# Optimization experiments

Hardware: AMD Instinct MI355X
Metric: run time of the kernel (lower is better)

The kernel has to match this reference:

```python
import jax, jax.numpy as jnp
import numpy as np

S, C, H, D = 4096, 2048, 16, 128  # seq, channels, heads, head_dim
EPS = 1.1920929e-07  # torch F.rms_norm default eps = finfo(float32).eps


def setup_inputs() -> dict:
    key = jax.random.key(0)
    ks = jax.random.split(key, 12)
    w = 0.02
    return {
        "x": jax.random.normal(ks[0], (S, C), dtype=jnp.float32),
        "rope": jax.random.normal(ks[1], (S, 1, D // 2, 2, 2), dtype=jnp.float32),
        "Wq": jax.random.normal(ks[2], (C, C), dtype=jnp.float32) * w,
        "bq": jnp.zeros((C,), dtype=jnp.float32),
        "Wk": jax.random.normal(ks[3], (C, C), dtype=jnp.float32) * w,
        "bk": jnp.zeros((C,), dtype=jnp.float32),
        "Wv": jax.random.normal(ks[4], (C, C), dtype=jnp.float32) * w,
        "bv": jnp.zeros((C,), dtype=jnp.float32),
        "qn_w": jnp.ones((D,), dtype=jnp.float32),
        "kn_w": jnp.ones((D,), dtype=jnp.float32),
        "Wo": jax.random.normal(ks[5], (C, C), dtype=jnp.float32) * w,
        "bo": jnp.zeros((C,), dtype=jnp.float32),
    }


def _rms_norm(x, weight):
    # RMSNorm over last dim, as F.rms_norm
    inv = jax.lax.rsqrt(jnp.mean(x * x, axis=-1, keepdims=True) + EPS)
    return x * inv * weight


def _apply_rotary(x, rope):
    # x: [S, H, D]; rope: [S, 1, D//2, 2, 2]
    s, h, d = x.shape
    x_ = x.reshape(s, h, d // 2, 1, 2)
    out = (rope * x_).sum(axis=-1)  # [S, H, D//2, 2]
    return out.reshape(s, h, d)


def reference(x, rope, Wq, bq, Wk, bk, Wv, bv, qn_w, kn_w, Wo, bo):
    # QKV projections -> [S, H, D]
    q = (x @ Wq.T + bq).reshape(S, H, D)
    k = (x @ Wk.T + bk).reshape(S, H, D)
    v = (x @ Wv.T + bv).reshape(S, H, D)
    # RMSNorm on q/k per head_dim
    q = _rms_norm(q, qn_w)
    k = _rms_norm(k, kn_w)
    # Custom rotary (table-driven 2x2 rotation)
    q = _apply_rotary(q, rope)
    k = _apply_rotary(k, rope)
    # Dense scaled dot-product attention over seq, per head
    scale = 1.0 / jnp.sqrt(jnp.asarray(D, dtype=q.dtype))
    scores = jnp.einsum("shd,thd->hst", q, k) * scale  # [H, S, S]
    probs = jax.nn.softmax(scores, axis=-1)
    out = jnp.einsum("hst,thd->shd", probs, v).reshape(S, C)
    return out @ Wo.T + bo
```

## Files before the change

kernel.cpp:

```cpp
#include <hip/hip_runtime.h>

#define S 4096
#define C 2048
#define H 16
#define D 128
#define EPS 1.1920929e-07f
#define QSCALE (0.08838834764831845f * 1.4426950408889634f)
#define BN 64
#define NT (S / BN)

typedef __attribute__((ext_vector_type(8))) short short8;
typedef __attribute__((ext_vector_type(4))) float f32x4;
typedef __attribute__((ext_vector_type(4))) unsigned int uint4v;

#if __has_builtin(__builtin_amdgcn_exp2f)
#define EXP2F __builtin_amdgcn_exp2f
#else
#define EXP2F exp2f
#endif

__device__ __forceinline__ unsigned short f2bf(float f) {
  unsigned int u = __builtin_bit_cast(unsigned int, f);
  u += 0x7fff + ((u >> 16) & 1);
  return (unsigned short)(u >> 16);
}
__device__ __forceinline__ float bf2f(unsigned short v) {
  unsigned int u = ((unsigned int)v) << 16;
  return __builtin_bit_cast(float, u);
}
__device__ __forceinline__ unsigned int pkbf(float a, float b) {
  return (unsigned int)f2bf(a) | ((unsigned int)f2bf(b) << 16);
}
__device__ __forceinline__ unsigned int pkbf_trunc(float a, float b) {
  return __builtin_amdgcn_perm(__builtin_bit_cast(unsigned int, b),
                               __builtin_bit_cast(unsigned int, a), 0x07060302);
}
__device__ __forceinline__ void gld16(const unsigned short* g, unsigned short* l) {
  __builtin_amdgcn_global_load_lds(
      (const __attribute__((address_space(1))) unsigned int*)g,
      (__attribute__((address_space(3))) unsigned int*)l, 16, 0, 0);
}
__device__ __forceinline__ short8 mk_a(unsigned int a, unsigned int b,
                                       unsigned int c, unsigned int d) {
  uint4v u;
  u[0] = a; u[1] = b; u[2] = c; u[3] = d;
  return __builtin_bit_cast(short8, u);
}

__global__ void cvt_kernel(const float* __restrict__ src,
                           unsigned short* __restrict__ dst, int n) {
  int i = (blockIdx.x * 256 + threadIdx.x) * 4;
  if (i >= n) return;
  float4 v = *(const float4*)(src + i);
  ushort4 o;
  o.x = f2bf(v.x); o.y = f2bf(v.y); o.z = f2bf(v.z); o.w = f2bf(v.w);
  *(ushort4*)(dst + i) = o;
}
__global__ void cvtw_kernel(const float* __restrict__ w0, const float* __restrict__ w1,
                            const float* __restrict__ w2, const float* __restrict__ w3,
                            unsigned short* __restrict__ dst) {
  const float* srcs[4] = {w0, w1, w2, w3};
  const float* src = srcs[blockIdx.y];
  int i = (blockIdx.x * 256 + threadIdx.x) * 4;
  float4 v = *(const float4*)(src + i);
  ushort4 o;
  o.x = f2bf(v.x); o.y = f2bf(v.y); o.z = f2bf(v.z); o.w = f2bf(v.w);
  *(ushort4*)(dst + (size_t)blockIdx.y * C * C + i) = o;
}
__global__ void bias_concat(const float* __restrict__ bq, const float* __restrict__ bk,
                            const float* __restrict__ bv, float* __restrict__ dst) {
  int i = blockIdx.x * 256 + threadIdx.x;
  const float* s = (i < C) ? bq : ((i < 2 * C) ? bk : bv);
  dst[i] = s[i & (C - 1)];
}

__global__ __launch_bounds__(256) void gemm_bt(const unsigned short* __restrict__ A,
                                               const unsigned short* __restrict__ B,
                                               const float* __restrict__ bias,
                                               float* __restrict__ outf,
                                               unsigned short* __restrict__ qh,
                                               unsigned short* __restrict__ kh,
                                               unsigned short* __restrict__ vt,
                                               int N, int mode) {
  __shared__ __align__(16) unsigned short U[128 * 136];
  unsigned short* Al = U;
  unsigned short* Bl = U + 128 * 64;
  const int t = threadIdx.x, w = t >> 6, lane = t & 63;
  const int lq = lane & 15, quad = lane >> 4;
  const int wm = w & 1, wn = w >> 1;
  const int m0 = blockIdx.y * 128, n0 = blockIdx.x * 128;
  f32x4 acc[4][4] = {};
  float biasv[4];
#pragma unroll
  for (int nt = 0; nt < 4; nt++) biasv[nt] = bias[n0 + wn * 64 + nt * 16 + lq];
  const int sr = lane >> 3, sg = lane & 7;
  for (int k0 = 0; k0 < C; k0 += 64) {
    __syncthreads();
#pragma unroll
    for (int p = 0; p < 4; p++) {
      int row = w * 32 + p * 8 + sr;
      int c = sg ^ (row & 7);
      gld16(A + (size_t)(m0 + row) * C + k0 + c * 8, &Al[(w * 32 + p * 8) * 64]);
      gld16(B + (size_t)(n0 + row) * C + k0 + c * 8, &Bl[(w * 32 + p * 8) * 64]);
    }
    __syncthreads();
#pragma unroll
    for (int ks = 0; ks < 2; ks++) {
      short8 af[4], bf[4];
#pragma unroll
      for (int mt = 0; mt < 4; mt++) {
        int row = wm * 64 + mt * 16 + lq;
        af[mt] = *(const short8*)&Al[row * 64 + ((ks * 4 + quad) ^ (lq & 7)) * 8];
      }
#pragma unroll
      for (int nt = 0; nt < 4; nt++) {
        int row = wn * 64 + nt * 16 + lq;
        bf[nt] = *(const short8*)&Bl[row * 64 + ((ks * 4 + quad) ^ (lq & 7)) * 8];
      }
#pragma unroll
      for (int mt = 0; mt < 4; mt++)
#pragma unroll
        for (int nt = 0; nt < 4; nt++)
          acc[mt][nt] = __builtin_amdgcn_mfma_f32_16x16x32_bf16(af[mt], bf[nt], acc[mt][nt], 0, 0, 0);
    }
  }

  if (mode == 0) {
#pragma unroll
    for (int mt = 0; mt < 4; mt++)
#pragma unroll
      for (int nt = 0; nt < 4; nt++) {
        int n = n0 + wn * 64 + nt * 16 + lq;
#pragma unroll
        for (int r = 0; r < 4; r++) {
          int m = m0 + wm * 64 + mt * 16 + quad * 4 + r;
          outf[(size_t)m * N + n] = acc[mt][nt][r] + biasv[nt];
        }
      }
    return;
  }

  const int gh = n0 >> 7;
  __syncthreads();
  const int rr = t >> 4, ck = t & 15;
  if (gh < 32) {
#pragma unroll
    for (int mt = 0; mt < 4; mt++)
#pragma unroll
      for (int nt = 0; nt < 4; nt++) {
        int dloc = wn * 64 + nt * 16 + lq;
#pragma unroll
        for (int r = 0; r < 4; r++)
          U[(wm * 64 + mt * 16 + quad * 4 + r) * 136 + dloc] = f2bf(acc[mt][nt][r] + biasv[nt]);
      }
    __syncthreads();
    unsigned short* dst = ((gh < 16) ? qh : kh) + (size_t)(gh & 15) * S * D;
#pragma unroll
    for (int p = 0; p < 8; p++) {
      int m = p * 16 + rr;
      uint4 vv = *(const uint4*)&U[m * 136 + ck * 8];
      *(uint4*)(dst + (size_t)(m0 + m) * D + ck * 8) = vv;
    }
  } else {
    #pragma unroll
    for (int mt = 0; mt < 4; mt++)
#pragma unroll
      for (int nt = 0; nt < 4; nt++) {
        int dloc = wn * 64 + nt * 16 + lq;
        int mlocP = wm * 64 + (mt >> 1) * 32 + quad * 8 + (mt & 1) * 4;
        *(unsigned int*)&U[dloc * 136 + mlocP] =
            pkbf(acc[mt][nt][0] + biasv[nt], acc[mt][nt][1] + biasv[nt]);
        *(unsigned int*)&U[dloc * 136 + mlocP + 2] =
            pkbf(acc[mt][nt][2] + biasv[nt], acc[mt][nt][3] + biasv[nt]);
      }
    __syncthreads();
    unsigned short* dst = vt + (size_t)(gh - 32) * D * S;
#pragma unroll
    for (int p = 0; p < 8; p++) {
      int d = p * 16 + rr;
      uint4 vv = *(const uint4*)&U[d * 136 + ck * 8];
      *(uint4*)(dst + (size_t)d * S + m0 + ck * 8) = vv;
    }
  }
}

__global__ __launch_bounds__(256) void rmsrope_kernel(unsigned short* __restrict__ qh,
                                                      unsigned short* __restrict__ kh,
                                                      const float* __restrict__ qn_w,
                                                      const float* __restrict__ kn_w,
                                                      const float* __restrict__ rope) {
  const int which = blockIdx.y;
  unsigned short* io = which ? kh : qh;
  const float* wgt = which ? kn_w : qn_w;
  const float scale = which ? 1.0f : QSCALE;
  int wid = (blockIdx.x * 256 + threadIdx.x) >> 6;
  int lane = threadIdx.x & 63;
  int s = wid & (S - 1);
  unsigned short* row = io + (size_t)wid * D;
  unsigned int pr = *(unsigned int*)(row + lane * 2);
  float a = bf2f((unsigned short)(pr & 0xffff));
  float b = bf2f((unsigned short)(pr >> 16));
  float ss = a * a + b * b;
  for (int m = 1; m < 64; m <<= 1) ss += __shfl_xor(ss, m);
  float inv = rsqrtf(ss * (1.0f / 128.0f) + EPS) * scale;
  float2 wv = *(const float2*)(wgt + lane * 2);
  float an = a * inv * wv.x, bn = b * inv * wv.y;
  float4 r = *(const float4*)(rope + (size_t)s * 256 + lane * 4);
  *(unsigned int*)(row + lane * 2) = pkbf(r.x * an + r.y * bn, r.z * an + r.w * bn);
}

__global__ __launch_bounds__(256, 2) void flash_kernel(const unsigned short* __restrict__ qh,
                                                       const unsigned short* __restrict__ kh,
                                                       const unsigned short* __restrict__ vt,
                                                       unsigned short* __restrict__ ao) {
  __shared__ __align__(16) unsigned short Klds[2 * BN * D];
  __shared__ __align__(16) unsigned short Vlds[2 * D * BN];
  const int h = blockIdx.y, i0 = blockIdx.x * 128;
  const int t = threadIdx.x, w = t >> 6, lane = t & 63;
  const int lq = lane & 15, quad = lane >> 4;

  const unsigned short* Qbase = qh + ((size_t)h * S + i0 + w * 32 + lq) * D;
  short8 qfrag[2][4];
#pragma unroll
  for (int qi = 0; qi < 2; qi++)
#pragma unroll
    for (int kt = 0; kt < 4; kt++)
      qfrag[qi][kt] = *(const short8*)(Qbase + (size_t)qi * 16 * D + kt * 32 + quad * 8);

  f32x4 oacc[2][8] = {};
  f32x4 dacc[2] = {};
  const unsigned short* Kbase = kh + (size_t)h * S * D;
  const unsigned short* Vbase = vt + (size_t)h * D * S;

  const int k_r = lane >> 4, k_g = lane & 15;
  const int v_r = lane >> 3, v_g = lane & 7;

  uint4v onesu;
  onesu[0] = 0x3F803F80u; onesu[1] = 0x3F803F80u; onesu[2] = 0x3F803F80u; onesu[3] = 0x3F803F80u;
  const short8 ones = __builtin_bit_cast(short8, onesu);

#pragma unroll
  for (int p = 0; p < 4; p++) {
    int kr = w * 16 + p * 4 + k_r;
    gld16(Kbase + (size_t)kr * D + (k_g ^ (kr & 7)) * 8, &Klds[(w * 16 + p * 4) * D]);
  }
#pragma unroll
  for (int p = 0; p < 4; p++) {
    int vr = w * 32 + p * 8 + v_r;
    gld16(Vbase + (size_t)vr * S + (v_g ^ (vr & 7)) * 8, &Vlds[(w * 32 + p * 8) * BN]);
  }

  for (int tt = 0; tt < NT; ++tt) {
    const int cur = tt & 1;
    unsigned short* Kc = Klds + cur * (BN * D);
    unsigned short* Vc = Vlds + cur * (D * BN);
    __syncthreads();
    if (tt + 1 < NT) {
      const int j1 = (tt + 1) * BN;
      unsigned short* Kn = Klds + (cur ^ 1) * (BN * D);
      unsigned short* Vn = Vlds + (cur ^ 1) * (D * BN);
#pragma unroll
      for (int p = 0; p < 4; p++) {
        int kr = w * 16 + p * 4 + k_r;
        gld16(Kbase + (size_t)(j1 + kr) * D + (k_g ^ (kr & 7)) * 8, &Kn[(w * 16 + p * 4) * D]);
      }
#pragma unroll
      for (int p = 0; p < 4; p++) {
        int vr = w * 32 + p * 8 + v_r;
        gld16(Vbase + (size_t)vr * S + j1 + (v_g ^ (vr & 7)) * 8, &Vn[(w * 32 + p * 8) * BN]);
      }
    }

    f32x4 sacc[2][4] = {};
    __builtin_amdgcn_s_setprio(1);
#pragma unroll
    for (int kt = 0; kt < 4; kt++)
#pragma unroll
      for (int nt = 0; nt < 4; nt++) {
        int row = nt * 16 + lq;
        short8 af = *(const short8*)&Kc[row * D + (((kt * 4 + quad) ^ (row & 7)) * 8)];
        sacc[0][nt] = __builtin_amdgcn_mfma_f32_16x16x32_bf16(af, qfrag[0][kt], sacc[0][nt], 0, 0, 0);
        sacc[1][nt] = __builtin_amdgcn_mfma_f32_16x16x32_bf16(af, qfrag[1][kt], sacc[1][nt], 0, 0, 0);
      }
    __builtin_amdgcn_s_setprio(0);

    unsigned int pd[2][4][2];
#pragma unroll
    for (int qi = 0; qi < 2; qi++)
#pragma unroll
      for (int nt = 0; nt < 4; nt++) {
        float e0 = EXP2F(sacc[qi][nt][0]);
        float e1 = EXP2F(sacc[qi][nt][1]);
        float e2 = EXP2F(sacc[qi][nt][2]);
        float e3 = EXP2F(sacc[qi][nt][3]);
        pd[qi][nt][0] = pkbf_trunc(e0, e1);
        pd[qi][nt][1] = pkbf_trunc(e2, e3);
      }

    __builtin_amdgcn_s_setprio(1);
#pragma unroll
    for (int kk = 0; kk < 2; kk++) {
      short8 a0 = mk_a(pd[0][2 * kk][0], pd[0][2 * kk][1], pd[0][2 * kk + 1][0], pd[0][2 * kk + 1][1]);
      short8 a1 = mk_a(pd[1][2 * kk][0], pd[1][2 * kk][1], pd[1][2 * kk + 1][0], pd[1][2 * kk + 1][1]);
      dacc[0] = __builtin_amdgcn_mfma_f32_16x16x32_bf16(a0, ones, dacc[0], 0, 0, 0);
      dacc[1] = __builtin_amdgcn_mfma_f32_16x16x32_bf16(a1, ones, dacc[1], 0, 0, 0);
#pragma unroll
      for (int dt = 0; dt < 8; dt++) {
        int row = dt * 16 + lq;
        short8 bf = *(const short8*)&Vc[row * BN + (((kk * 4 + quad) ^ (row & 7)) * 8)];
        oacc[0][dt] = __builtin_amdgcn_mfma_f32_16x16x32_bf16(a0, bf, oacc[0][dt], 0, 0, 0);
        oacc[1][dt] = __builtin_amdgcn_mfma_f32_16x16x32_bf16(a1, bf, oacc[1][dt], 0, 0, 0);
      }
    }
    __builtin_amdgcn_s_setprio(0);
  }

  float il[2][4];
#pragma unroll
  for (int qi = 0; qi < 2; qi++)
#pragma unroll
    for (int r = 0; r < 4; r++) il[qi][r] = 1.0f / dacc[qi][r];
#pragma unroll
  for (int qi = 0; qi < 2; qi++)
#pragma unroll
    for (int dt = 0; dt < 8; dt++)
#pragma unroll
      for (int r = 0; r < 4; r++)
        ao[(size_t)(i0 + w * 32 + qi * 16 + quad * 4 + r) * C + h * 128 + dt * 16 + lq] =
            f2bf(oacc[qi][dt][r] * il[qi][r]);
}

extern "C" void kernel_launch(void* const* d_in, const int* in_sizes, int n_in,
                              void* d_out, int out_size, void* d_ws, size_t ws_size,
                              hipStream_t stream) {
  const float* x    = (const float*)d_in[0];
  const float* rope = (const float*)d_in[1];
  const float* Wq   = (const float*)d_in[2];
  const float* bq   = (const float*)d_in[3];
  const float* Wk   = (const float*)d_in[4];
  const float* bk   = (const float*)d_in[5];
  const float* Wv   = (const float*)d_in[6];
  const float* bv   = (const float*)d_in[7];
  const float* qn_w = (const float*)d_in[8];
  const float* kn_w = (const float*)d_in[9];
  const float* Wo   = (const float*)d_in[10];
  const float* bo   = (const float*)d_in[11];
  float* out = (float*)d_out;

  unsigned short* xb  = (unsigned short*)d_ws;
  unsigned short* wqb = xb + (size_t)S * C;
  unsigned short* wob = wqb + (size_t)3 * C * C;
  unsigned short* qh  = wqb + (size_t)4 * C * C;
  unsigned short* kh  = qh + (size_t)S * C;
  unsigned short* vt  = kh + (size_t)S * C;
  unsigned short* ao  = vt + (size_t)S * C;
  float* bqkv = (float*)(ao + (size_t)S * C);

  cvt_kernel<<<S * C / 1024, 256, 0, stream>>>(x, xb, S * C);
  cvtw_kernel<<<dim3(C * C / 1024, 4), 256, 0, stream>>>(Wq, Wk, Wv, Wo, wqb);
  bias_concat<<<3 * C / 256, 256, 0, stream>>>(bq, bk, bv, bqkv);

  gemm_bt<<<dim3(3 * C / 128, S / 128), 256, 0, stream>>>(
      xb, wqb, bqkv, nullptr, qh, kh, vt, 3 * C, 1);

  rmsrope_kernel<<<dim3((H * S) / 4, 2), 256, 0, stream>>>(qh, kh, qn_w, kn_w, rope);

  flash_kernel<<<dim3(S / 128, H), 256, 0, stream>>>(qh, kh, vt, ao);

  gemm_bt<<<dim3(C / 128, S / 128), 256, 0, stream>>>(
      ao, wob, bo, out, nullptr, nullptr, nullptr, C, 0);
}
```

Baseline: 463.6 us.

## Triple-buffer GEMM with larger 256x128 tiles, 512 threads, and XCD-aware block remap

Rewrites the projection GEMM to use 256x128 tiles with 8 waves and a three-stage LDS ring, fed by async global-to-LDS loads and gated by vmcnt waits so loads for later K tiles overlap the MFMA work on the current one. Block IDs are remapped to group work across the 8 XCDs for better L2 reuse, and s_setprio is raised around the MFMA burst. The epilogues are adjusted to the taller tile. LDS use grows to about 144KB per block, which limits occupancy, and the explicit vmcnt counts depend on how many loads the compiler emits per stage.

```diff
diff --git a/kernel.cpp b/kernel.cpp
--- a/kernel.cpp
+++ b/kernel.cpp
@@ -8,6 +8,11 @@
 #define QSCALE (0.08838834764831845f * 1.4426950408889634f)
 #define BN 64
 #define NT (S / BN)
+#define GBM 256
+#define GBN 128
+#define GBK 64
+#define NKT (C / GBK)
+#define GBUF (GBM * GBK + GBN * GBK)
 
 typedef __attribute__((ext_vector_type(8))) short short8;
 typedef __attribute__((ext_vector_type(4))) float f32x4;
@@ -74,55 +79,91 @@
   dst[i] = s[i & (C - 1)];
 }
 
-__global__ __launch_bounds__(256) void gemm_bt(const unsigned short* __restrict__ A,
-                                               const unsigned short* __restrict__ B,
-                                               const float* __restrict__ bias,
-                                               float* __restrict__ outf,
-                                               unsigned short* __restrict__ qh,
-                                               unsigned short* __restrict__ kh,
-                                               unsigned short* __restrict__ vt,
-                                               int N, int mode) {
-  __shared__ __align__(16) unsigned short U[128 * 136];
-  unsigned short* Al = U;
-  unsigned short* Bl = U + 128 * 64;
+__global__ __launch_bounds__(512, 2) void gemm_bt(const unsigned short* __restrict__ A,
+                                                  const unsigned short* __restrict__ B,
+                                                  const float* __restrict__ bias,
+                                                  float* __restrict__ outf,
+                                                  unsigned short* __restrict__ qh,
+                                                  unsigned short* __restrict__ kh,
+                                                  unsigned short* __restrict__ vt,
+                                                  int N, int mode) {
+  __shared__ __align__(16) unsigned short L[3 * GBUF];
   const int t = threadIdx.x, w = t >> 6, lane = t & 63;
   const int lq = lane & 15, quad = lane >> 4;
-  const int wm = w & 1, wn = w >> 1;
-  const int m0 = blockIdx.y * 128, n0 = blockIdx.x * 128;
+  const int wm = w >> 1, wn = w & 1;
+
+  const int nwg = gridDim.x * gridDim.y;
+  int id = blockIdx.x * gridDim.y + blockIdx.y;
+  int nid = (id & 7) * (nwg >> 3) + (id >> 3);
+  const int bx = nid / (int)gridDim.y, by = nid % (int)gridDim.y;
+  const int m0 = by * GBM, n0 = bx * GBN;
+
   f32x4 acc[4][4] = {};
   float biasv[4];
 #pragma unroll
   for (int nt = 0; nt < 4; nt++) biasv[nt] = bias[n0 + wn * 64 + nt * 16 + lq];
-  const int sr = lane >> 3, sg = lane & 7;
-  for (int k0 = 0; k0 < C; k0 += 64) {
-    __syncthreads();
+
+  const int srow = lane >> 3, sg = lane & 7;
+  auto stage = [&](int tt, int b) {
+    unsigned short* Ab = L + b * GBUF;
+    unsigned short* Bb = Ab + GBM * GBK;
+    const int k0 = tt * GBK;
 #pragma unroll
     for (int p = 0; p < 4; p++) {
-      int row = w * 32 + p * 8 + sr;
+      int row = p * 64 + w * 8 + srow;
       int c = sg ^ (row & 7);
-      gld16(A + (size_t)(m0 + row) * C + k0 + c * 8, &Al[(w * 32 + p * 8) * 64]);
-      gld16(B + (size_t)(n0 + row) * C + k0 + c * 8, &Bl[(w * 32 + p * 8) * 64]);
-    }
-    __syncthreads();
-#pragma unroll
-    for (int ks = 0; ks < 2; ks++) {
-      short8 af[4], bf[4];
-#pragma unroll
-      for (int mt = 0; mt < 4; mt++) {
-        int row = wm * 64 + mt * 16 + lq;
-        af[mt] = *(const short8*)&Al[row * 64 + ((ks * 4 + quad) ^ (lq & 7)) * 8];
-      }
-#pragma unroll
-      for (int nt = 0; nt < 4; nt++) {
-        int row = wn * 64 + nt * 16 + lq;
-        bf[nt] = *(const short8*)&Bl[row * 64 + ((ks * 4 + quad) ^ (lq & 7)) * 8];
-      }
+      gld16(A + (size_t)(m0 + row) * C + k0 + c * 8, Ab + (p * 64 + w * 8) * GBK);
+    }
+#pragma unroll
+    for (int p = 0; p < 2; p++) {
+      int row = p * 64 + w * 8 + srow;
+      int c = sg ^ (row & 7);
+      gld16(B + (size_t)(n0 + row) * C + k0 + c * 8, Bb + (p * 64 + w * 8) * GBK);
+    }
+  };
+
+  stage(0, 0);
+  stage(1, 1);
+
+  int cb = 0;
+  for (int tt = 0; tt < NKT; ++tt) {
+    if (tt < NKT - 1)
+      asm volatile("s_waitcnt vmcnt(6)" ::: "memory");
+    else
+      asm volatile("s_waitcnt vmcnt(0)" ::: "memory");
+    __builtin_amdgcn_s_barrier();
+    asm volatile("" ::: "memory");
+    if (tt + 2 < NKT) {
+      int sb = cb + 2; if (sb >= 3) sb -= 3;
+      stage(tt + 2, sb);
+    }
+    unsigned short* Ab = L + cb * GBUF;
+    unsigned short* Bb = Ab + GBM * GBK;
+    short8 af[4][2], bf[4][2];
+#pragma unroll
+    for (int mt = 0; mt < 4; mt++) {
+      int row = wm * 64 + mt * 16 + lq;
+#pragma unroll
+      for (int ks = 0; ks < 2; ks++)
+        af[mt][ks] = *(const short8*)&Ab[row * GBK + (((ks * 4 + quad) ^ (row & 7)) * 8)];
+    }
+#pragma unroll
+    for (int nt = 0; nt < 4; nt++) {
+      int row = wn * 64 + nt * 16 + lq;
+#pragma unroll
+      for (int ks = 0; ks < 2; ks++)
+        bf[nt][ks] = *(const short8*)&Bb[row * GBK + (((ks * 4 + quad) ^ (row & 7)) * 8)];
+    }
+    __builtin_amdgcn_s_setprio(1);
+#pragma unroll
+    for (int ks = 0; ks < 2; ks++)
 #pragma unroll
       for (int mt = 0; mt < 4; mt++)
 #pragma unroll
         for (int nt = 0; nt < 4; nt++)
-          acc[mt][nt] = __builtin_amdgcn_mfma_f32_16x16x32_bf16(af[mt], bf[nt], acc[mt][nt], 0, 0, 0);
-    }
+          acc[mt][nt] = __builtin_amdgcn_mfma_f32_16x16x32_bf16(af[mt][ks], bf[nt][ks], acc[mt][nt], 0, 0, 0);
+    __builtin_amdgcn_s_setprio(0);
+    cb = (cb == 2) ? 0 : cb + 1;
   }
 
   if (mode == 0) {
@@ -140,10 +181,10 @@
     return;
   }
 
-  const int gh = n0 >> 7;
+  const int gh = bx;
   __syncthreads();
-  const int rr = t >> 4, ck = t & 15;
   if (gh < 32) {
+    unsigned short* U = L;
 #pragma unroll
     for (int mt = 0; mt < 4; mt++)
 #pragma unroll
@@ -155,30 +196,33 @@
       }
     __syncthreads();
     unsigned short* dst = ((gh < 16) ? qh : kh) + (size_t)(gh & 15) * S * D;
+    const int rr = t >> 4, ck = t & 15;
 #pragma unroll
     for (int p = 0; p < 8; p++) {
-      int m = p * 16 + rr;
+      int m = p * 32 + rr;
       uint4 vv = *(const uint4*)&U[m * 136 + ck * 8];
       *(uint4*)(dst + (size_t)(m0 + m) * D + ck * 8) = vv;
     }
   } else {
-    #pragma unroll
+    unsigned short* U = L;
+#pragma unroll
     for (int mt = 0; mt < 4; mt++)
 #pragma unroll
       for (int nt = 0; nt < 4; nt++) {
         int dloc = wn * 64 + nt * 16 + lq;
         int mlocP = wm * 64 + (mt >> 1) * 32 + quad * 8 + (mt & 1) * 4;
-        *(unsigned int*)&U[dloc * 136 + mlocP] =
+        *(unsigned int*)&U[dloc * 264 + mlocP] =
             pkbf(acc[mt][nt][0] + biasv[nt], acc[mt][nt][1] + biasv[nt]);
-        *(unsigned int*)&U[dloc * 136 + mlocP + 2] =
+        *(unsigned int*)&U[dloc * 264 + mlocP + 2] =
             pkbf(acc[mt][nt][2] + biasv[nt], acc[mt][nt][3] + biasv[nt]);
       }
     __syncthreads();
     unsigned short* dst = vt + (size_t)(gh - 32) * D * S;
+    const int rr = t >> 5, ck = t & 31;
 #pragma unroll
     for (int p = 0; p < 8; p++) {
       int d = p * 16 + rr;
-      uint4 vv = *(const uint4*)&U[d * 136 + ck * 8];
+      uint4 vv = *(const uint4*)&U[d * 264 + ck * 8];
       *(uint4*)(dst + (size_t)d * S + m0 + ck * 8) = vv;
     }
   }
@@ -360,13 +404,13 @@
   cvtw_kernel<<<dim3(C * C / 1024, 4), 256, 0, stream>>>(Wq, Wk, Wv, Wo, wqb);
   bias_concat<<<3 * C / 256, 256, 0, stream>>>(bq, bk, bv, bqkv);
 
-  gemm_bt<<<dim3(3 * C / 128, S / 128), 256, 0, stream>>>(
+  gemm_bt<<<dim3(3 * C / GBN, S / GBM), 512, 0, stream>>>(
       xb, wqb, bqkv, nullptr, qh, kh, vt, 3 * C, 1);
 
   rmsrope_kernel<<<dim3((H * S) / 4, 2), 256, 0, stream>>>(qh, kh, qn_w, kn_w, rope);
 
   flash_kernel<<<dim3(S / 128, H), 256, 0, stream>>>(qh, kh, vt, ao);
 
-  gemm_bt<<<dim3(C / 128, S / 128), 256, 0, stream>>>(
+  gemm_bt<<<dim3(C / GBN, S / GBM), 512, 0, stream>>>(
       ao, wob, bo, out, nullptr, nullptr, nullptr, C, 0);
 }
```

Result: faster. 439.9 us (-5.1%).
